# Performance work log

Measured on AMD Instinct MI355X. Metric: run time of the kernel, lower is better.

Reference implementation:

```python
import jax, jax.numpy as jnp
import numpy as np

D_MODEL = 1024
N_HEADS = 16
HEAD_DIM = 64
INNER = N_HEADS * HEAD_DIM
ROPE_BASE = 10000.0


def _rope(q, k):
    # q, k: [b, h, s, d]; standard half-split rotary embedding, fraction=1.0
    s, d = q.shape[-2], q.shape[-1]
    inv_freq = 1.0 / (ROPE_BASE ** (jnp.arange(0, d, 2, dtype=jnp.float32) / d))
    freqs = jnp.arange(s, dtype=jnp.float32)[:, None] * inv_freq[None, :]  # [s, d/2]
    cos = jnp.concatenate([jnp.cos(freqs), jnp.cos(freqs)], axis=-1)  # [s, d]
    sin = jnp.concatenate([jnp.sin(freqs), jnp.sin(freqs)], axis=-1)

    def rot_half(x):
        x1, x2 = x[..., : d // 2], x[..., d // 2:]
        return jnp.concatenate([-x2, x1], axis=-1)

    q = q * cos + rot_half(q) * sin
    k = k * cos + rot_half(k) * sin
    return q, k


def _heads(x, W):
    # x: [b, s, d_model], W: [d_model, inner] -> [b, h, s, hd]
    b, s, _ = x.shape
    y = x @ W
    return y.reshape(b, s, N_HEADS, HEAD_DIM).transpose(0, 2, 1, 3)


def setup_inputs() -> dict:
    key = jax.random.key(0)
    ks = jax.random.split(key, 10)
    B, S = 8, 512
    std = D_MODEL ** -0.5
    inp = {
        "x": jax.random.normal(ks[0], (B, S, D_MODEL), dtype=jnp.float32),
        "chain_ids": jax.random.randint(ks[1], (B, S), 0, 2, dtype=jnp.int32),
        "attention_mask": jnp.ones((B, S), dtype=bool),
        "Wq_self": jax.random.normal(ks[2], (D_MODEL, INNER), jnp.float32) * std,
        "Wk_self": jax.random.normal(ks[3], (D_MODEL, INNER), jnp.float32) * std,
        "Wv_self": jax.random.normal(ks[4], (D_MODEL, INNER), jnp.float32) * std,
        "Wq_cross": jax.random.normal(ks[5], (D_MODEL, INNER), jnp.float32) * std,
        "Wk_cross": jax.random.normal(ks[6], (D_MODEL, INNER), jnp.float32) * std,
        "Wv_cross": jax.random.normal(ks[7], (D_MODEL, INNER), jnp.float32) * std,
        "Wo": jax.random.normal(ks[8], (INNER, D_MODEL), jnp.float32) * (INNER ** -0.5),
    }
    return inp


def reference(x, chain_ids, attention_mask, Wq_self, Wk_self, Wv_self,
              Wq_cross, Wk_cross, Wv_cross, Wo):
    b, s, _ = x.shape
    scale = HEAD_DIM ** -0.5

    q_s, k_s, v_s = _heads(x, Wq_self), _heads(x, Wk_self), _heads(x, Wv_self)
    q_c, k_c, v_c = _heads(x, Wq_cross), _heads(x, Wk_cross), _heads(x, Wv_cross)
    q_s, k_s = _rope(q_s, k_s)

    scores_self = jnp.einsum('bhqd,bhkd->bhqk', q_s, k_s) * scale
    scores_cross = jnp.einsum('bhqd,bhkd->bhqk', q_c, k_c) * scale

    # intra-chain mask: [b, 1, s, s]
    intra = (chain_ids[:, None, :, None] == chain_ids[:, None, None, :])
    merged = jnp.where(intra, scores_self, scores_cross)

    # additive padding mask: -inf where key is padding
    pad = jnp.where(attention_mask, 0.0, -jnp.inf)[:, None, None, :]
    merged = merged + pad

    attn = jax.nn.softmax(merged, axis=-1)
    attn = jnp.nan_to_num(attn, nan=0.0)

    intra_f = intra.astype(x.dtype)
    out_self = jnp.einsum('bhqk,bhkd->bhqd', attn * intra_f, v_s)
    out_cross = jnp.einsum('bhqk,bhkd->bhqd', attn * (1.0 - intra_f), v_c)
    out = (out_self + out_cross).transpose(0, 2, 1, 3).reshape(b, s, INNER)
    return out @ Wo
```

## Files before the change

kernel.cpp:

```cpp
#include <hip/hip_runtime.h>
#include <math.h>


#define NB 8
#define NS 512
#define ND 1024
#define NH 16
#define NDH 64
#define ATT_SCALE 0.125f

typedef _Float16 half_t;
typedef _Float16 half8 __attribute__((ext_vector_type(8)));
typedef float f32x4 __attribute__((ext_vector_type(4)));
typedef float f32x16 __attribute__((ext_vector_type(16)));

#define MFMA16(a, b, c) __builtin_amdgcn_mfma_f32_16x16x32_f16(a, b, c, 0, 0, 0)
#define MFMA32(a, b, c) __builtin_amdgcn_mfma_f32_32x32x16_f16(a, b, c, 0, 0, 0)

__device__ __forceinline__ void gl2lds16(const half_t* g, half_t* l) {
  __builtin_amdgcn_global_load_lds(
      (const __attribute__((address_space(1))) unsigned int*)(const void*)g,
      (__attribute__((address_space(3))) unsigned int*)(void*)l, 16, 0, 0);
}

struct WIn { const float* W[7]; };
struct GemmOuts { half_t* O[6]; };

__global__ __launch_bounds__(256) void prep_kernel(const float* __restrict__ x,
                                                   half_t* __restrict__ x16,
                                                   WIn win,
                                                   half_t* __restrict__ WT) {
  const int lin = blockIdx.x;
  const int tid = threadIdx.x;
  if (lin < 2048) {
    const size_t i = ((size_t)lin * 256 + tid) * 8;
    float4 a = *(const float4*)&x[i];
    float4 b = *(const float4*)&x[i + 4];
    half8 h;
    h[0] = (half_t)a.x; h[1] = (half_t)a.y; h[2] = (half_t)a.z;
    h[3] = (half_t)a.w; h[4] = (half_t)b.x; h[5] = (half_t)b.y;
    h[6] = (half_t)b.z; h[7] = (half_t)b.w;
    *(half8*)&x16[i] = h;
    return;
  }
  __shared__ float T[64][65];
  const int t = lin - 2048;
  const int z = t >> 8;
  const int tile = t & 255;
  const int tx = tile & 15, ty = tile >> 4;
  const float* W = win.W[z];
  half_t* dst = WT + (size_t)z * ND * ND;
#pragma unroll
  for (int i = 0; i < 4; ++i) {
    const int r = (tid >> 4) + 16 * i;
    const int c0 = (tid & 15) * 4;
    float4 v = *(const float4*)&W[(size_t)(ty * 64 + r) * ND + tx * 64 + c0];
    T[r][c0] = v.x; T[r][c0 + 1] = v.y; T[r][c0 + 2] = v.z; T[r][c0 + 3] = v.w;
  }
  __syncthreads();
#pragma unroll
  for (int it = 0; it < 2; ++it) {
    const int slot = tid + 256 * it;
    const int n = slot >> 3;
    const int k0 = (slot & 7) * 8;
    half8 h;
#pragma unroll
    for (int j = 0; j < 8; ++j) h[j] = (half_t)T[k0 + j][n];
    *(half8*)&dst[(size_t)(tx * 64 + n) * ND + ty * 64 + k0] = h;
  }
}

#define G16_BUF 24576

__global__ __launch_bounds__(512, 2) void gemm16_kernel(
    const half_t* __restrict__ A, const half_t* __restrict__ WT,
    GemmOuts outs) {
  __shared__ __align__(16) half_t SMEM[3 * G16_BUF];

  const int lin = blockIdx.x;
  const int bx = lin & 7;
  const int z = (lin >> 3) % 6;
  const int by = lin / 48;

  const int tid = threadIdx.x;
  const int wave = tid >> 6;
  const int lane = tid & 63;
  const int m16 = lane & 15;
  const int g = lane >> 4;
  const int wr = wave >> 1;
  const int wc = wave & 1;
  const int kk = (m16 >> 1) & 3;

  const half_t* W = WT + (size_t)z * ND * ND;
  const int row0 = by * 256;
  const int col0 = bx * 128;

  const int swz = ((lane & 3) ^ ((lane >> 3) & 3)) * 8;
  const int rowsel = lane >> 2;
  const half_t* gsrc[6];
  int ldst[6];
#pragma unroll
  for (int s = 0; s < 6; ++s) {
    const int seg = wave * 6 + s;
    if (seg < 32) {
      const int kk2 = seg >> 4, rg = seg & 15;
      gsrc[s] = A + (size_t)(row0 + rg * 16 + rowsel) * ND + kk2 * 32 + swz;
      ldst[s] = kk2 * 8192 + rg * 512;
    } else {
      const int s2 = seg - 32, kk2 = s2 >> 3, rg = s2 & 7;
      gsrc[s] = W + (size_t)(col0 + rg * 16 + rowsel) * ND + kk2 * 32 + swz;
      ldst[s] = 16384 + kk2 * 4096 + rg * 512;
    }
  }

  f32x4 acc[4][4] = {};

#define G_STAGE3(t, p)                                                   \
  {                                                                      \
    half_t* sb_ = SMEM + ((t) % 3) * G16_BUF;                            \
    _Pragma("unroll") for (int s_ = (p) * 3; s_ < (p) * 3 + 3; ++s_)     \
        gl2lds16(gsrc[s_] + (size_t)(t) * 64, sb_ + ldst[s_]);           \
  }

#define G_PHASE(cb, kk2, DOSTAGE, t)                                         \
  {                                                                          \
    half8 af[4], bf[4];                                                      \
    const half_t* Ab_ = (cb) + (kk2) * 8192;                                 \
    const half_t* Bb_ = (cb) + 16384 + (kk2) * 4096;                         \
    _Pragma("unroll") for (int i = 0; i < 4; ++i) af[i] =                    \
        *(const half8*)&Ab_[(wr * 64 + i * 16 + m16) * 32 + (g ^ kk) * 8];   \
    _Pragma("unroll") for (int j = 0; j < 4; ++j) bf[j] =                    \
        *(const half8*)&Bb_[(wc * 64 + j * 16 + m16) * 32 + (g ^ kk) * 8];   \
    if (DOSTAGE) G_STAGE3((t) + 2, kk2);                                     \
    __builtin_amdgcn_s_barrier();                                            \
    asm volatile("s_waitcnt lgkmcnt(0)" ::: "memory");                       \
    __builtin_amdgcn_s_setprio(1);                                           \
    _Pragma("unroll") for (int i = 0; i < 4; ++i)                            \
        _Pragma("unroll") for (int j = 0; j < 4; ++j)                        \
            acc[i][j] = MFMA16(af[i], bf[j], acc[i][j]);                     \
    __builtin_amdgcn_s_setprio(0);                                           \
  }

#pragma unroll
  for (int s = 0; s < 6; ++s) gl2lds16(gsrc[s], SMEM + ldst[s]);
#pragma unroll
  for (int s = 0; s < 6; ++s)
    gl2lds16(gsrc[s] + 64, SMEM + G16_BUF + ldst[s]);
  asm volatile("s_waitcnt vmcnt(6)" ::: "memory");
  __builtin_amdgcn_s_barrier();

  for (int t = 0; t < 14; ++t) {
    half_t* cb = SMEM + (t % 3) * G16_BUF;
    G_PHASE(cb, 0, true, t);
    __builtin_amdgcn_s_barrier();
    G_PHASE(cb, 1, true, t);
    asm volatile("s_waitcnt vmcnt(6)" ::: "memory");
    __builtin_amdgcn_s_barrier();
  }
  {
    half_t* cb = SMEM + (14 % 3) * G16_BUF;
    G_PHASE(cb, 0, false, 14);
    __builtin_amdgcn_s_barrier();
    G_PHASE(cb, 1, false, 14);
    asm volatile("s_waitcnt vmcnt(0)" ::: "memory");
    __builtin_amdgcn_s_barrier();
  }
  {
    half_t* cb = SMEM + (15 % 3) * G16_BUF;
    G_PHASE(cb, 0, false, 15);
    __builtin_amdgcn_s_barrier();
    G_PHASE(cb, 1, false, 15);
    asm volatile("s_waitcnt lgkmcnt(0)" ::: "memory");
    __builtin_amdgcn_s_barrier();
  }

  half_t* O = outs.O[z];
  const int h = (col0 + wc * 64) >> 6;

  if (z == 2 || z == 5) {
    const int rbase = row0 + wr * 64;
    const int b = rbase >> 9;
    const int s0 = rbase & (NS - 1);
    half_t* dst = O + (size_t)(b * NH + h) * NDH * NS;
    half_t* T = SMEM + wave * 4608;
#pragma unroll
    for (int i = 0; i < 4; ++i)
#pragma unroll
      for (int j = 0; j < 4; ++j)
#pragma unroll
        for (int rr = 0; rr < 4; ++rr)
          T[(j * 16 + m16) * 72 + (i * 16 + g * 4 + rr)] =
              (half_t)acc[i][j][rr];
#pragma unroll
    for (int it = 0; it < 8; ++it) {
      const int slot = lane + 64 * it;
      const int d = slot >> 3;
      const int sl = (slot & 7) * 8;
      half8 v = *(const half8*)&T[d * 72 + sl];
      *(half8*)&dst[(size_t)d * NS + s0 + sl] = v;
    }
    return;
  }

  const bool rope = (z == 0 || z == 1);
  float invf0 = 0.f, invf1 = 0.f;
  if (rope) {
    const float c0 = -logf(10000.0f) / 32.0f;
    invf0 = __expf((float)(m16) * c0);
    invf1 = __expf((float)(16 + m16) * c0);
  }
#pragma unroll
  for (int i = 0; i < 4; ++i) {
    const int r = row0 + wr * 64 + i * 16 + g * 4;
#pragma unroll
    for (int rr = 0; rr < 4; ++rr) {
      const int rg = r + rr;
      const int b = rg >> 9;
      const int s = rg & (NS - 1);
      half_t* orow = O + ((size_t)(b * NH + h) * NS + s) * NDH;
      float v0 = acc[i][0][rr], v1 = acc[i][1][rr];
      float v2 = acc[i][2][rr], v3 = acc[i][3][rr];
      if (rope) {
        float sn, cs;
        __sincosf((float)s * invf0, &sn, &cs);
        const float n0 = v0 * cs - v2 * sn;
        const float n2 = v2 * cs + v0 * sn;
        __sincosf((float)s * invf1, &sn, &cs);
        const float n1 = v1 * cs - v3 * sn;
        const float n3 = v3 * cs + v1 * sn;
        v0 = n0; v1 = n1; v2 = n2; v3 = n3;
      }
      orow[0 * 16 + m16] = (half_t)v0;
      orow[1 * 16 + m16] = (half_t)v1;
      orow[2 * 16 + m16] = (half_t)v2;
      orow[3 * 16 + m16] = (half_t)v3;
    }
  }
}

__global__ __launch_bounds__(256, 2) void outgemm_kernel(
    const half_t* __restrict__ A, const half_t* __restrict__ W,
    float* __restrict__ Cout) {
  __shared__ __align__(16) half_t SMEM[6144];
  half_t* As = SMEM;
  half_t* Bs = SMEM + 4096;

  const int tid = threadIdx.x;
  const int wave = tid >> 6;
  const int lane = tid & 63;
  const int m16 = lane & 15;
  const int g = lane >> 4;

  const int row0 = blockIdx.y * 128;
  const int col0 = blockIdx.x * 64;
  const int wy = wave >> 1;
  const int wx = wave & 1;

  const int sa_m = wave * 32 + (lane >> 2);
  const int sb_m = wave * 16 + (lane >> 2);
  const int sa_k = ((lane & 3) ^ ((lane >> 3) & 3)) * 8;
  const int kk = (m16 >> 1) & 3;

  f32x4 acc[4][2] = {};
  for (int k0 = 0; k0 < ND; k0 += 32) {
    __syncthreads();
    gl2lds16(A + (size_t)(row0 + sa_m) * ND + k0 + sa_k,
             &As[(wave * 2 + 0) * 512]);
    gl2lds16(A + (size_t)(row0 + sa_m + 16) * ND + k0 + sa_k,
             &As[(wave * 2 + 1) * 512]);
    gl2lds16(W + (size_t)(col0 + sb_m) * ND + k0 + sa_k, &Bs[wave * 512]);
    __syncthreads();
    half8 af[4], bf[2];
#pragma unroll
    for (int i = 0; i < 4; ++i)
      af[i] = *(const half8*)&As[(wy * 64 + i * 16 + m16) * 32 + (g ^ kk) * 8];
#pragma unroll
    for (int j = 0; j < 2; ++j)
      bf[j] = *(const half8*)&Bs[(wx * 32 + j * 16 + m16) * 32 + (g ^ kk) * 8];
#pragma unroll
    for (int i = 0; i < 4; ++i)
#pragma unroll
      for (int j = 0; j < 2; ++j) acc[i][j] = MFMA16(af[i], bf[j], acc[i][j]);
  }

  float* FT = (float*)SMEM;
  for (int round = 0; round < 4; ++round) {
    __syncthreads();
    if (wave != round) continue;
#pragma unroll
    for (int i = 0; i < 4; ++i)
#pragma unroll
      for (int j = 0; j < 2; ++j)
#pragma unroll
        for (int rr = 0; rr < 4; ++rr)
          FT[(i * 16 + g * 4 + rr) * 36 + j * 16 + m16] = acc[i][j][rr];
#pragma unroll
    for (int it = 0; it < 8; ++it) {
      const int slot = lane + 64 * it;
      const int lr = slot >> 3;
      const int c4 = (slot & 7) * 4;
      float4 v = *(const float4*)&FT[lr * 36 + c4];
      *(float4*)&Cout[(size_t)(row0 + wy * 64 + lr) * ND + col0 + wx * 32 + c4] =
          v;
    }
  }
}

__global__ __launch_bounds__(256, 2) void attn_kernel(
    const half_t* __restrict__ qs, const half_t* __restrict__ ks,
    const half_t* __restrict__ vs, const half_t* __restrict__ qc,
    const half_t* __restrict__ kc, const half_t* __restrict__ vc,
    const int* __restrict__ chain, half_t* __restrict__ ao) {
  __shared__ half_t KS[64 * 64], KC[64 * 64], VS[64 * 64], VC[64 * 64];
  __shared__ half_t P4[4][32 * 72];
  __shared__ int ck[NS];
  __shared__ unsigned int mbits[128 * 17];

  const int tid = threadIdx.x;
  const int wave = tid >> 6;
  const int lane = tid & 63;
  const int m32 = lane & 31;
  const int g2 = lane >> 5;
  const int bh = blockIdx.x & 127;
  const int b = bh >> 4;
  const int h = bh & 15;
  const int q0 = (blockIdx.x >> 7) * 128;
  const size_t base = (size_t)bh * NS * NDH;

  ck[tid] = chain[b * NS + tid];
  ck[tid + 256] = chain[b * NS + tid + 256];
  __syncthreads();

  {
    const int w = tid & 15, qg = tid >> 4;
    int cqv[8];
    unsigned int bits[8];
#pragma unroll
    for (int r = 0; r < 8; ++r) {
      cqv[r] = ck[q0 + qg * 8 + r];
      bits[r] = 0u;
    }
    for (int j = 0; j < 32; ++j) {
      const int ckj = ck[w * 32 + j];
#pragma unroll
      for (int r = 0; r < 8; ++r)
        if (ckj == cqv[r]) bits[r] |= (1u << j);
    }
#pragma unroll
    for (int r = 0; r < 8; ++r) mbits[(qg * 8 + r) * 17 + w] = bits[r];
  }

  half8 aS[4], aC[4];
  {
    const size_t qoff = base + (size_t)(q0 + wave * 32 + m32) * NDH + g2 * 8;
#pragma unroll
    for (int c = 0; c < 4; ++c) {
      aS[c] = *(const half8*)&qs[qoff + c * 16];
      aC[c] = *(const half8*)&qc[qoff + c * 16];
    }
  }
  int cqr[16];
#pragma unroll
  for (int reg = 0; reg < 16; ++reg) {
    const int row = (reg & 3) + 8 * (reg >> 2) + 4 * g2;
    cqr[reg] = ck[q0 + wave * 32 + row];
  }

  float sums[16];
#pragma unroll
  for (int r = 0; r < 16; ++r) sums[r] = 0.f;
  f32x16 accO[2] = {};

  half_t* PW = &P4[wave][0];
  const int goffK = (lane >> 3) * NDH + (((lane & 7) ^ (lane >> 3)) << 3);
  const int goffV = (lane >> 3) * NS + (((lane & 7) ^ (lane >> 3)) << 3);

  for (int kt = 0; kt < 8; ++kt) {
    const int kb = kt * 64;
    __syncthreads();
    if (wave == 0) {
#pragma unroll
      for (int j = 0; j < 8; ++j)
        gl2lds16(ks + base + (size_t)(kb + j * 8) * NDH + goffK,
                 &KS[j * 8 * 64]);
    } else if (wave == 1) {
#pragma unroll
      for (int j = 0; j < 8; ++j)
        gl2lds16(kc + base + (size_t)(kb + j * 8) * NDH + goffK,
                 &KC[j * 8 * 64]);
    } else if (wave == 2) {
#pragma unroll
      for (int j = 0; j < 8; ++j)
        gl2lds16(vs + base + (size_t)(j * 8) * NS + kb + goffV,
                 &VS[j * 8 * 64]);
    } else {
#pragma unroll
      for (int j = 0; j < 8; ++j)
        gl2lds16(vc + base + (size_t)(j * 8) * NS + kb + goffV,
                 &VC[j * 8 * 64]);
    }
    __syncthreads();

    const unsigned int mw0 = mbits[(wave * 32 + m32) * 17 + kt * 2];
    const unsigned int mw1 = mbits[(wave * 32 + m32) * 17 + kt * 2 + 1];

#pragma unroll
    for (int kt2 = 0; kt2 < 2; ++kt2) {
      const int key = kt2 * 32 + m32;
      const int k7 = key & 7;
      f32x16 cS = {};
      f32x16 cC = {};
#pragma unroll
      for (int c = 0; c < 4; ++c) {
        const int cc = (c * 2 + g2) ^ k7;
        half8 bS = *(const half8*)&KS[(key * 8 + cc) * 8];
        half8 bC = *(const half8*)&KC[(key * 8 + cc) * 8];
        cS = MFMA32(aS[c], bS, cS);
        cC = MFMA32(aC[c], bC, cC);
      }
      const int ckk = ck[kb + key];
#pragma unroll
      for (int reg = 0; reg < 16; ++reg) {
        const float sel = (ckk == cqr[reg]) ? cS[reg] : cC[reg];
        const float e = __expf(fmaf(sel, ATT_SCALE, -4.0f));
        sums[reg] += e;
        const int row = (reg & 3) + 8 * (reg >> 2) + 4 * g2;
        PW[row * 72 + kt2 * 32 + m32] = (half_t)e;
      }
    }

#pragma unroll
    for (int c = 0; c < 4; ++c) {
      half8 pf = *(const half8*)&PW[m32 * 72 + c * 16 + g2 * 8];
      const unsigned int w32 = (c < 2) ? mw0 : mw1;
      const unsigned int mb = (w32 >> ((c & 1) * 16 + g2 * 8)) & 0xffu;
      half8 psf;
#pragma unroll
      for (int j = 0; j < 8; ++j)
        psf[j] = ((mb >> j) & 1u) ? pf[j] : (half_t)0.f;
      half8 pcf = pf - psf;
#pragma unroll
      for (int dt = 0; dt < 2; ++dt) {
        const int d = dt * 32 + m32;
        const int cc = (c * 2 + g2) ^ (d & 7);
        half8 bs = *(const half8*)&VS[(d * 8 + cc) * 8];
        half8 bc = *(const half8*)&VC[(d * 8 + cc) * 8];
        accO[dt] = MFMA32(psf, bs, accO[dt]);
        accO[dt] = MFMA32(pcf, bc, accO[dt]);
      }
    }
  }

#pragma unroll
  for (int reg = 0; reg < 16; ++reg) {
    float s = sums[reg];
#pragma unroll
    for (int off = 1; off < 32; off <<= 1) s += __shfl_xor(s, off);
    sums[reg] = 1.0f / s;
  }

#pragma unroll
  for (int dt = 0; dt < 2; ++dt)
#pragma unroll
    for (int reg = 0; reg < 16; ++reg) {
      const int row = (reg & 3) + 8 * (reg >> 2) + 4 * g2;
      const int qg = q0 + wave * 32 + row;
      ao[(size_t)(b * NS + qg) * ND + h * NDH + dt * 32 + m32] =
          (half_t)(accO[dt][reg] * sums[reg]);
    }
}

extern "C" void kernel_launch(void* const* d_in, const int* in_sizes, int n_in,
                              void* d_out, int out_size, void* d_ws,
                              size_t ws_size, hipStream_t stream) {
  const float* x = (const float*)d_in[0];
  const int* chain = (const int*)d_in[1];
  float* out = (float*)d_out;

  half_t* ws = (half_t*)d_ws;
  const size_t M = (size_t)NB * NH * NS * NDH;
  half_t* x16 = ws;
  half_t* WT = x16 + M;
  half_t* q_s = WT + (size_t)7 * ND * ND;
  half_t* k_s = q_s + M;
  half_t* v_s = k_s + M;
  half_t* q_c = v_s + M;
  half_t* k_c = q_c + M;
  half_t* v_c = k_c + M;
  half_t* ao = v_c + M;

  WIn win;
  for (int i = 0; i < 7; ++i) win.W[i] = (const float*)d_in[3 + i];
  GemmOuts go;
  go.O[0] = q_s; go.O[1] = k_s; go.O[2] = v_s;
  go.O[3] = q_c; go.O[4] = k_c; go.O[5] = v_c;

  hipLaunchKernelGGL(prep_kernel, dim3(3840), dim3(256), 0, stream, x, x16,
                     win, WT);
  hipLaunchKernelGGL(gemm16_kernel, dim3(768), dim3(512), 0, stream, x16,
                     WT, go);
  hipLaunchKernelGGL(attn_kernel, dim3(512), dim3(256), 0, stream, q_s,
                     k_s, v_s, q_c, k_c, v_c, chain, ao);
  hipLaunchKernelGGL(outgemm_kernel, dim3(16, 32), dim3(256), 0, stream, ao,
                     WT + (size_t)6 * ND * ND, out);
}
```

Baseline: 218.5 us.

## Load K/V fragments directly from global memory into registers in attention

The attention kernel no longer stages K and V tiles through shared memory with global_load_lds and two block barriers per key tile. Each wave now reads its K and V MFMA operand fragments straight from global memory (L2/L1) into registers, and one barrier is added after mask setup. This removes the LDS staging, the barriers and the LDS footprint, which may raise occupancy. In exchange, all four waves now read the same K/V data from global memory separately, and load latency is exposed without explicit prefetch.

New measurement: 251.8 us. 15.3% more time.

```diff
diff --git a/kernel.cpp b/kernel.cpp
--- a/kernel.cpp
+++ b/kernel.cpp
@@ -311,7 +311,6 @@
     const half_t* __restrict__ vs, const half_t* __restrict__ qc,
     const half_t* __restrict__ kc, const half_t* __restrict__ vc,
     const int* __restrict__ chain, half_t* __restrict__ ao) {
-  __shared__ half_t KS[64 * 64], KC[64 * 64], VS[64 * 64], VC[64 * 64];
   __shared__ half_t P4[4][32 * 72];
   __shared__ int ck[NS];
   __shared__ unsigned int mbits[128 * 17];
@@ -349,6 +348,7 @@
 #pragma unroll
     for (int r = 0; r < 8; ++r) mbits[(qg * 8 + r) * 17 + w] = bits[r];
   }
+  __syncthreads();
 
   half8 aS[4], aC[4];
   {
@@ -372,34 +372,21 @@
   f32x16 accO[2] = {};
 
   half_t* PW = &P4[wave][0];
-  const int goffK = (lane >> 3) * NDH + (((lane & 7) ^ (lane >> 3)) << 3);
-  const int goffV = (lane >> 3) * NS + (((lane & 7) ^ (lane >> 3)) << 3);
 
   for (int kt = 0; kt < 8; ++kt) {
     const int kb = kt * 64;
-    __syncthreads();
-    if (wave == 0) {
-#pragma unroll
-      for (int j = 0; j < 8; ++j)
-        gl2lds16(ks + base + (size_t)(kb + j * 8) * NDH + goffK,
-                 &KS[j * 8 * 64]);
-    } else if (wave == 1) {
-#pragma unroll
-      for (int j = 0; j < 8; ++j)
-        gl2lds16(kc + base + (size_t)(kb + j * 8) * NDH + goffK,
-                 &KC[j * 8 * 64]);
-    } else if (wave == 2) {
-#pragma unroll
-      for (int j = 0; j < 8; ++j)
-        gl2lds16(vs + base + (size_t)(j * 8) * NS + kb + goffV,
-                 &VS[j * 8 * 64]);
-    } else {
-#pragma unroll
-      for (int j = 0; j < 8; ++j)
-        gl2lds16(vc + base + (size_t)(j * 8) * NS + kb + goffV,
-                 &VC[j * 8 * 64]);
-    }
-    __syncthreads();
+
+    half8 vSf[2][4], vCf[2][4];
+#pragma unroll
+    for (int dt = 0; dt < 2; ++dt) {
+      const half_t* vrowS = vs + base + (size_t)(dt * 32 + m32) * NS + kb;
+      const half_t* vrowC = vc + base + (size_t)(dt * 32 + m32) * NS + kb;
+#pragma unroll
+      for (int c = 0; c < 4; ++c) {
+        vSf[dt][c] = *(const half8*)&vrowS[(c * 2 + g2) * 8];
+        vCf[dt][c] = *(const half8*)&vrowC[(c * 2 + g2) * 8];
+      }
+    }
 
     const unsigned int mw0 = mbits[(wave * 32 + m32) * 17 + kt * 2];
     const unsigned int mw1 = mbits[(wave * 32 + m32) * 17 + kt * 2 + 1];
@@ -407,14 +394,14 @@
 #pragma unroll
     for (int kt2 = 0; kt2 < 2; ++kt2) {
       const int key = kt2 * 32 + m32;
-      const int k7 = key & 7;
+      const half_t* krowS = ks + base + (size_t)(kb + key) * NDH;
+      const half_t* krowC = kc + base + (size_t)(kb + key) * NDH;
       f32x16 cS = {};
       f32x16 cC = {};
 #pragma unroll
       for (int c = 0; c < 4; ++c) {
-        const int cc = (c * 2 + g2) ^ k7;
-        half8 bS = *(const half8*)&KS[(key * 8 + cc) * 8];
-        half8 bC = *(const half8*)&KC[(key * 8 + cc) * 8];
+        half8 bS = *(const half8*)&krowS[(c * 2 + g2) * 8];
+        half8 bC = *(const half8*)&krowC[(c * 2 + g2) * 8];
         cS = MFMA32(aS[c], bS, cS);
         cC = MFMA32(aC[c], bC, cC);
       }
@@ -441,12 +428,8 @@
       half8 pcf = pf - psf;
 #pragma unroll
       for (int dt = 0; dt < 2; ++dt) {
-        const int d = dt * 32 + m32;
-        const int cc = (c * 2 + g2) ^ (d & 7);
-        half8 bs = *(const half8*)&VS[(d * 8 + cc) * 8];
-        half8 bc = *(const half8*)&VC[(d * 8 + cc) * 8];
-        accO[dt] = MFMA32(psf, bs, accO[dt]);
-        accO[dt] = MFMA32(pcf, bc, accO[dt]);
+        accO[dt] = MFMA32(psf, vSf[dt][c], accO[dt]);
+        accO[dt] = MFMA32(pcf, vCf[dt][c], accO[dt]);
       }
     }
   }
```

## Double-buffer K tiles and overlap V loads with QK^T compute in attention

Applied to the files above, without the earlier changes.

K tiles for the self and cross branches move into a two-slot LDS buffer. The next tile is prefetched while the current one feeds the QK^T MFMAs, and V tile loads are issued before the score computation and waited on only before the PV stage. The two full __syncthreads per iteration become split barriers with explicit vmcnt/lgkmcnt waits. The goal is to hide global-to-LDS load latency behind compute, at the cost of extra LDS (one more K buffer pair) and hand-managed synchronisation that could race if the waits are wrong.

Result: slower. 224.9 us (+2.9%).

```diff
diff --git a/kernel.cpp b/kernel.cpp
--- a/kernel.cpp
+++ b/kernel.cpp
@@ -311,7 +311,8 @@
     const half_t* __restrict__ vs, const half_t* __restrict__ qc,
     const half_t* __restrict__ kc, const half_t* __restrict__ vc,
     const int* __restrict__ chain, half_t* __restrict__ ao) {
-  __shared__ half_t KS[64 * 64], KC[64 * 64], VS[64 * 64], VC[64 * 64];
+  __shared__ half_t KB[2][8192];
+  __shared__ half_t VS[64 * 64], VC[64 * 64];
   __shared__ half_t P4[4][32 * 72];
   __shared__ int ck[NS];
   __shared__ unsigned int mbits[128 * 17];
@@ -375,31 +376,49 @@
   const int goffK = (lane >> 3) * NDH + (((lane & 7) ^ (lane >> 3)) << 3);
   const int goffV = (lane >> 3) * NS + (((lane & 7) ^ (lane >> 3)) << 3);
 
+  if (wave == 0) {
+#pragma unroll
+    for (int j = 0; j < 8; ++j)
+      gl2lds16(ks + base + (size_t)(j * 8) * NDH + goffK, &KB[0][j * 512]);
+  } else if (wave == 1) {
+#pragma unroll
+    for (int j = 0; j < 8; ++j)
+      gl2lds16(kc + base + (size_t)(j * 8) * NDH + goffK,
+               &KB[0][4096 + j * 512]);
+  }
+  __syncthreads();
+
   for (int kt = 0; kt < 8; ++kt) {
     const int kb = kt * 64;
-    __syncthreads();
+    const half_t* Kcur = &KB[kt & 1][0];
+
     if (wave == 0) {
-#pragma unroll
-      for (int j = 0; j < 8; ++j)
-        gl2lds16(ks + base + (size_t)(kb + j * 8) * NDH + goffK,
-                 &KS[j * 8 * 64]);
+      if (kt < 7) {
+        half_t* kdst = &KB[(kt + 1) & 1][0];
+#pragma unroll
+        for (int j = 0; j < 8; ++j)
+          gl2lds16(ks + base + (size_t)(kb + 64 + j * 8) * NDH + goffK,
+                   kdst + j * 512);
+      }
     } else if (wave == 1) {
-#pragma unroll
-      for (int j = 0; j < 8; ++j)
-        gl2lds16(kc + base + (size_t)(kb + j * 8) * NDH + goffK,
-                 &KC[j * 8 * 64]);
+      if (kt < 7) {
+        half_t* kdst = &KB[(kt + 1) & 1][4096];
+#pragma unroll
+        for (int j = 0; j < 8; ++j)
+          gl2lds16(kc + base + (size_t)(kb + 64 + j * 8) * NDH + goffK,
+                   kdst + j * 512);
+      }
     } else if (wave == 2) {
 #pragma unroll
       for (int j = 0; j < 8; ++j)
         gl2lds16(vs + base + (size_t)(j * 8) * NS + kb + goffV,
-                 &VS[j * 8 * 64]);
+                 &VS[j * 512]);
     } else {
 #pragma unroll
       for (int j = 0; j < 8; ++j)
         gl2lds16(vc + base + (size_t)(j * 8) * NS + kb + goffV,
-                 &VC[j * 8 * 64]);
-    }
-    __syncthreads();
+                 &VC[j * 512]);
+    }
 
     const unsigned int mw0 = mbits[(wave * 32 + m32) * 17 + kt * 2];
     const unsigned int mw1 = mbits[(wave * 32 + m32) * 17 + kt * 2 + 1];
@@ -413,8 +432,8 @@
 #pragma unroll
       for (int c = 0; c < 4; ++c) {
         const int cc = (c * 2 + g2) ^ k7;
-        half8 bS = *(const half8*)&KS[(key * 8 + cc) * 8];
-        half8 bC = *(const half8*)&KC[(key * 8 + cc) * 8];
+        half8 bS = *(const half8*)&Kcur[(key * 8 + cc) * 8];
+        half8 bC = *(const half8*)&Kcur[4096 + (key * 8 + cc) * 8];
         cS = MFMA32(aS[c], bS, cS);
         cC = MFMA32(aC[c], bC, cC);
       }
@@ -428,6 +447,10 @@
         PW[row * 72 + kt2 * 32 + m32] = (half_t)e;
       }
     }
+
+    if (wave >= 2) asm volatile("s_waitcnt vmcnt(0)" ::: "memory");
+    __builtin_amdgcn_s_barrier();
+    __builtin_amdgcn_sched_barrier(0);
 
 #pragma unroll
     for (int c = 0; c < 4; ++c) {
@@ -449,6 +472,11 @@
         accO[dt] = MFMA32(pcf, bc, accO[dt]);
       }
     }
+
+    if (wave < 2) asm volatile("s_waitcnt vmcnt(0)" ::: "memory");
+    asm volatile("s_waitcnt lgkmcnt(0)" ::: "memory");
+    __builtin_amdgcn_s_barrier();
+    __builtin_amdgcn_sched_barrier(0);
   }
 
 #pragma unroll
```
